# Performance work log

Hardware: AMD Instinct MI355X
Metric: run time of the kernel (lower is better)

## Reference

```python
import jax, jax.numpy as jnp
import numpy as np

N = 100000   # num nodes
E = 1600000  # num edges
D = 64       # feature / hidden dim (irreps_in == hidden_dim)
SCALE = D ** -0.5


def setup_inputs() -> dict:
    key = jax.random.key(0)
    ks = jax.random.split(key, 6)
    x = jax.random.normal(ks[0], (N, D), dtype=jnp.float32)
    edge_index = jax.random.randint(ks[1], (2, E), 0, N, dtype=jnp.int32)
    std = D ** -0.5
    Wq = jax.random.normal(ks[2], (D, D), dtype=jnp.float32) * std
    Wk = jax.random.normal(ks[3], (D, D), dtype=jnp.float32) * std
    Wv = jax.random.normal(ks[4], (D, D), dtype=jnp.float32) * std
    Wo = jax.random.normal(ks[5], (D, D), dtype=jnp.float32) * std
    return {"x": x, "edge_index": edge_index, "Wq": Wq, "Wk": Wk, "Wv": Wv, "Wo": Wo}


def reference(x, edge_index, Wq, Wk, Wv, Wo):
    # Per-receiver variable-length attention over incoming neighbors.
    # Mathematically identical to the torch module's degree-bucketed SDPA
    # (softmax over each node's neighbor set), without padding buffers.
    sender, receiver = edge_index[0], edge_index[1]
    Q = x @ Wq  # [N, D]
    K = x @ Wk
    V = x @ Wv
    # per-edge logits: <Q[receiver], K[sender]> * scale
    s = jnp.einsum('ed,ed->e', Q[receiver], K[sender]) * SCALE  # [E]
    # numerically stable segment softmax over receiver groups
    m = jax.ops.segment_max(s, receiver, num_segments=N)  # -inf for empty segments
    m_safe = jnp.where(jnp.isfinite(m), m, 0.0)
    p = jnp.exp(s - m_safe[receiver])  # [E]
    denom = jax.ops.segment_sum(p, receiver, num_segments=N)  # [N]
    num = jax.ops.segment_sum(p[:, None] * V[sender], receiver, num_segments=N)  # [N, D]
    # zero-degree nodes get out = 0 (matches torch: skipped buckets + nan_to_num)
    out = jnp.where(denom[:, None] > 0,
                    num / jnp.maximum(denom, 1e-30)[:, None],
                    0.0)
    return x + out @ Wo
```

## Files before the change

kernel.cpp:

```cpp
#include <hip/hip_runtime.h>
#include <hip/hip_bf16.h>

#define DIM 64
#define SCALE 0.125f
#define BINSH 5
#define NPB 32
#define BCAP 768
#define CHUNK 16384
#define MAXBINS 3200

static __device__ __forceinline__ unsigned int pack2bf(float a, float b) {
    unsigned int ua = __float_as_uint(a), ub = __float_as_uint(b);
    ua += 0x7fffu + ((ua >> 16) & 1u);
    ub += 0x7fffu + ((ub >> 16) & 1u);
    return (ua >> 16) | (ub & 0xffff0000u);
}
static __device__ __forceinline__ float2 unpack2bf(unsigned int u) {
    return make_float2(__uint_as_float(u << 16), __uint_as_float(u & 0xffff0000u));
}

__global__ __launch_bounds__(256) void k_fused(const int* __restrict__ send,
                                               const int* __restrict__ recv,
                                               const float* __restrict__ x,
                                               const float* __restrict__ Wq,
                                               const float* __restrict__ Wk,
                                               const float* __restrict__ Wv,
                                               const float* __restrict__ Wo,
                                               int* __restrict__ binCur,
                                               unsigned int* __restrict__ ebufA,
                                               float* __restrict__ Q,
                                               unsigned int* __restrict__ KVb,
                                               int E, int N, int NBK,
                                               int NBIN, int nchunk) {
    __shared__ __align__(16) float smem[20480];
    int tid = threadIdx.x;

    if ((int)blockIdx.x < NBIN) {
        int* hist = (int*)smem;
        int* lcur = hist + MAXBINS;
        int base = blockIdx.x * CHUNK;
        int lim = min(base + CHUNK, E);

        for (int i = tid; i < NBK; i += 256) hist[i] = 0;
        __syncthreads();
        for (int i = base + tid; i < lim; i += 256)
            atomicAdd(&hist[recv[i] >> BINSH], 1);
        __syncthreads();
        for (int i = tid; i < NBK; i += 256) {
            int h = hist[i];
            lcur[i] = h ? atomicAdd(&binCur[i], h) : 0;
        }
        __syncthreads();
        for (int i = base + tid; i < lim; i += 256) {
            int r = recv[i];
            int b = r >> BINSH;
            int p = atomicAdd(&lcur[b], 1);
            if (p < BCAP)
                ebufA[(size_t)b * BCAP + p] =
                    (unsigned)send[i] | ((unsigned)(r & (NPB - 1)) << 17);
        }
        return;
    }

    float* ws = smem;
    float* xs = smem + 4096;
    int wv = tid >> 6;
    int lane = tid & 63;
    int qb = blockIdx.x - NBIN;
    int m = qb / nchunk;
    int cb = qb % nchunk;

    if (m < 2) {
        const float* W = (m == 0) ? Wq : Wk;
        for (int i = tid; i < 1024; i += 256) ((float4*)ws)[i] = ((const float4*)W)[i];
        __syncthreads();
    } else {
        float* av = xs;
        float* bo = xs + 4096;
        for (int i = tid; i < 1024; i += 256) {
            ((float4*)av)[i] = ((const float4*)Wv)[i];
            ((float4*)bo)[i] = ((const float4*)Wo)[i];
        }
        __syncthreads();
        int r = tid >> 2, c0 = (tid & 3) * 16;
        float wvo[16];
#pragma unroll
        for (int j = 0; j < 16; j++) wvo[j] = 0.f;
        for (int k = 0; k < 64; k++) {
            float a = av[r * 64 + k];
#pragma unroll
            for (int j = 0; j < 16; j++)
                wvo[j] = fmaf(a, bo[k * 64 + c0 + j], wvo[j]);
        }
        __syncthreads();
#pragma unroll
        for (int j = 0; j < 16; j++) ws[r * 64 + c0 + j] = wvo[j];
        __syncthreads();
    }

    int base = cb * 256 + wv * 64;
    if (base < N) {
        float* xw = xs + wv * 4096;
#pragma unroll
        for (int c4 = 0; c4 < 16; c4++) {
            float4 v = make_float4(0.f, 0.f, 0.f, 0.f);
            if (base + lane < N) v = ((const float4*)x)[(size_t)(base + lane) * 16 + c4];
            xw[(c4 * 4 + 0) * 64 + lane] = v.x;
            xw[(c4 * 4 + 1) * 64 + lane] = v.y;
            xw[(c4 * 4 + 2) * 64 + lane] = v.z;
            xw[(c4 * 4 + 3) * 64 + lane] = v.w;
        }
        asm volatile("s_waitcnt lgkmcnt(0)" ::: "memory");

        int lr = lane >> 3;
        int lc = lane & 7;
        const float* xp = xw + lr * 8;
        const float* wp = ws + lc * 8;

        float acc[8][8];
#pragma unroll
        for (int i = 0; i < 8; i++)
#pragma unroll
            for (int j = 0; j < 8; j++) acc[i][j] = 0.f;

        float4 xa = *(const float4*)(xp);
        float4 xb = *(const float4*)(xp + 4);
        float4 wa = *(const float4*)(wp);
        float4 wb = *(const float4*)(wp + 4);
#pragma unroll 4
        for (int k = 0; k < 64; k++) {
            float4 xan, xbn, wan, wbn;
            if (k < 63) {
                xan = *(const float4*)(xp + (k + 1) * 64);
                xbn = *(const float4*)(xp + (k + 1) * 64 + 4);
                wan = *(const float4*)(wp + (k + 1) * 64);
                wbn = *(const float4*)(wp + (k + 1) * 64 + 4);
            }
            float xv[8] = {xa.x, xa.y, xa.z, xa.w, xb.x, xb.y, xb.z, xb.w};
            float wc[8] = {wa.x, wa.y, wa.z, wa.w, wb.x, wb.y, wb.z, wb.w};
#pragma unroll
            for (int i = 0; i < 8; i++)
#pragma unroll
                for (int j = 0; j < 8; j++)
                    acc[i][j] = fmaf(xv[i], wc[j], acc[i][j]);
            xa = xan; xb = xbn; wa = wan; wb = wbn;
        }

#pragma unroll
        for (int i = 0; i < 8; i++) {
            int row = base + lr * 8 + i;
            if (row < N) {
                if (m == 0) {
                    float* dst = &Q[(size_t)row * 64 + lc * 8];
                    ((float4*)dst)[0] = make_float4(acc[i][0], acc[i][1], acc[i][2], acc[i][3]);
                    ((float4*)dst)[1] = make_float4(acc[i][4], acc[i][5], acc[i][6], acc[i][7]);
                } else {
                    unsigned int* dst = &KVb[(size_t)row * 64 + (m - 1) * 32 + lc * 4];
                    uint4 pk;
                    pk.x = pack2bf(acc[i][0], acc[i][1]);
                    pk.y = pack2bf(acc[i][2], acc[i][3]);
                    pk.z = pack2bf(acc[i][4], acc[i][5]);
                    pk.w = pack2bf(acc[i][6], acc[i][7]);
                    *((uint4*)dst) = pk;
                }
            }
        }
    }
}

__global__ __launch_bounds__(256) void k_attn(const float* __restrict__ Q,
                                              const unsigned int* __restrict__ KVb,
                                              const float* __restrict__ x,
                                              const int* __restrict__ binCur,
                                              const unsigned int* __restrict__ ebufA,
                                              float* __restrict__ out, int N) {
    __shared__ unsigned int llist[BCAP];
    __shared__ int ldeg[NPB], lofs[NPB + 1], lcur[NPB];
    int tid = threadIdx.x;
    int wv = tid >> 6;
    int lane = tid & 63;
    int g = lane >> 3;
    int sub = lane & 7;

    int j = blockIdx.x;
    int cnt = min(binCur[j], BCAP);
    const unsigned int* ebin = ebufA + (size_t)j * BCAP;

    if (tid < NPB) ldeg[tid] = 0;
    __syncthreads();

    for (int i = tid; i < cnt; i += 256)
        atomicAdd(&ldeg[(ebin[i] >> 17) & (NPB - 1)], 1);
    __syncthreads();

    if (wv == 0 && lane < NPB) {
        int d = ldeg[lane];
        int s = d;
        for (int o = 1; o < NPB; o <<= 1) {
            int t = __shfl_up(s, o, NPB);
            if ((lane & (NPB - 1)) >= o) s += t;
        }
        lofs[lane + 1] = s;
        lcur[lane] = s - d;
        if (lane == 0) lofs[0] = 0;
    }
    __syncthreads();

    for (int i = tid; i < cnt; i += 256) {
        unsigned int u = ebin[i];
        int n = (u >> 17) & (NPB - 1);
        int p = atomicAdd(&lcur[n], 1);
        llist[p] = u & 0x1FFFFu;
    }
    __syncthreads();

    for (int n = wv; n < NPB; n += 4) {
        int r = (j << BINSH) + n;
        if (r >= N) break;
        int start = lofs[n];
        int end = lofs[n + 1];
        float4 qa = *((const float4*)&Q[(size_t)r * 64 + sub * 8]);
        float4 qb = *((const float4*)&Q[(size_t)r * 64 + sub * 8 + 4]);
        float q[8] = {qa.x, qa.y, qa.z, qa.w, qb.x, qb.y, qb.z, qb.w};
        float acc[8] = {0.f, 0.f, 0.f, 0.f, 0.f, 0.f, 0.f, 0.f};
        float dpart = 0.f;

        int eA = start + g;
        bool vA = eA < end;
        unsigned int sA = vA ? llist[eA] : 0u;
        uint4 kA = *((const uint4*)&KVb[(size_t)sA * 64 + sub * 4]);
        uint4 uA = *((const uint4*)&KVb[(size_t)sA * 64 + 32 + sub * 4]);
        int eB = start + 8 + g;
        bool vB = eB < end;
        unsigned int sB = vB ? llist[eB] : 0u;
        uint4 kB = *((const uint4*)&KVb[(size_t)sB * 64 + sub * 4]);
        uint4 uB = *((const uint4*)&KVb[(size_t)sB * 64 + 32 + sub * 4]);

        for (int bb = start; bb < end; bb += 8) {
            int eC = bb + 16 + g;
            bool vC = eC < end;
            unsigned int sC = vC ? llist[eC] : 0u;
            uint4 kC = *((const uint4*)&KVb[(size_t)sC * 64 + sub * 4]);
            uint4 uC = *((const uint4*)&KVb[(size_t)sC * 64 + 32 + sub * 4]);

            float2 k01 = unpack2bf(kA.x), k23 = unpack2bf(kA.y);
            float2 k45 = unpack2bf(kA.z), k67 = unpack2bf(kA.w);
            float dot = q[0] * k01.x + q[1] * k01.y + q[2] * k23.x + q[3] * k23.y
                      + q[4] * k45.x + q[5] * k45.y + q[6] * k67.x + q[7] * k67.y;
            dot += __shfl_xor(dot, 1);
            dot += __shfl_xor(dot, 2);
            dot += __shfl_xor(dot, 4);
            float w = vA ? __expf(dot * SCALE) : 0.f;

            float2 v01 = unpack2bf(uA.x), v23 = unpack2bf(uA.y);
            float2 v45 = unpack2bf(uA.z), v67 = unpack2bf(uA.w);
            acc[0] = fmaf(w, v01.x, acc[0]);
            acc[1] = fmaf(w, v01.y, acc[1]);
            acc[2] = fmaf(w, v23.x, acc[2]);
            acc[3] = fmaf(w, v23.y, acc[3]);
            acc[4] = fmaf(w, v45.x, acc[4]);
            acc[5] = fmaf(w, v45.y, acc[5]);
            acc[6] = fmaf(w, v67.x, acc[6]);
            acc[7] = fmaf(w, v67.y, acc[7]);
            dpart += w;

            kA = kB; uA = uB; vA = vB;
            kB = kC; uB = uC; vB = vC;
        }

        dpart += __shfl_xor(dpart, 8); dpart += __shfl_xor(dpart, 16); dpart += __shfl_xor(dpart, 32);
#pragma unroll
        for (int jj = 0; jj < 8; jj++) {
            acc[jj] += __shfl_xor(acc[jj], 8);
            acc[jj] += __shfl_xor(acc[jj], 16);
            acc[jj] += __shfl_xor(acc[jj], 32);
        }

        float inv = (dpart > 0.f) ? (1.0f / dpart) : 0.f;

        if (g == 0) {
            float4 xa = *((const float4*)&x[(size_t)r * 64 + sub * 8]);
            float4 xb = *((const float4*)&x[(size_t)r * 64 + sub * 8 + 4]);
            float4 oa = make_float4(fmaf(acc[0], inv, xa.x), fmaf(acc[1], inv, xa.y),
                                    fmaf(acc[2], inv, xa.z), fmaf(acc[3], inv, xa.w));
            float4 ob = make_float4(fmaf(acc[4], inv, xb.x), fmaf(acc[5], inv, xb.y),
                                    fmaf(acc[6], inv, xb.z), fmaf(acc[7], inv, xb.w));
            *((float4*)&out[(size_t)r * 64 + sub * 8]) = oa;
            *((float4*)&out[(size_t)r * 64 + sub * 8 + 4]) = ob;
        }
    }
}


extern "C" void kernel_launch(void* const* d_in, const int* in_sizes, int n_in,
                              void* d_out, int out_size, void* d_ws, size_t ws_size,
                              hipStream_t stream) {
    const float* x  = (const float*)d_in[0];
    const int* edge = (const int*)d_in[1];
    const float* Wq = (const float*)d_in[2];
    const float* Wk = (const float*)d_in[3];
    const float* Wv = (const float*)d_in[4];
    const float* Wo = (const float*)d_in[5];
    float* out = (float*)d_out;

    int N = in_sizes[0] / DIM;
    int E = in_sizes[1] / 2;
    int NBK = (N + NPB - 1) >> BINSH;

    char* p = (char*)d_ws;
    auto cv = [&](size_t bytes) {
        char* r = p;
        p += ((bytes + 255) / 256) * 256;
        return r;
    };
    float*        Q      = (float*)cv((size_t)N * 64 * 4);
    unsigned int* KVb    = (unsigned int*)cv((size_t)N * 64 * 4);
    int*          binCur = (int*)cv((size_t)NBK * 4);
    unsigned int* ebufA  = (unsigned int*)cv((size_t)NBK * BCAP * 4);
    (void)ws_size; (void)n_in; (void)out_size;

    const int* send = edge;
    const int* recv = edge + E;

    int NBIN = (E + CHUNK - 1) / CHUNK;
    int nchunk = (N + 255) / 256;

    hipMemsetAsync(binCur, 0, (size_t)NBK * 4, stream);
    k_fused<<<NBIN + 3 * nchunk, 256, 0, stream>>>(send, recv, x, Wq, Wk, Wv, Wo,
                                                   binCur, ebufA, Q, KVb,
                                                   E, N, NBK, NBIN, nchunk);
    k_attn<<<NBK, 256, 0, stream>>>(Q, KVb, x, binCur, ebufA, out, N);
}
```

Measured before the change: 241.7 us.

## Precompute Wv@Wo in separate kernel and read weights from global in projection

Moves the per-block Wv·Wo product into a single tiny kernel that runs once, instead of having every V-projection block recompute it. Projection blocks now read weight rows directly from global/L2, with a two-deep register prefetch, rather than staging them in shared memory. This cuts LDS per block from 80KB to 64KB. The binning chunk size is also halved to spread histogramming over more blocks. The trade-offs are an extra kernel launch and global-latency weight reads in the inner loop.

```diff
diff --git a/kernel.cpp b/kernel.cpp
--- a/kernel.cpp
+++ b/kernel.cpp
@@ -6,7 +6,7 @@
 #define BINSH 5
 #define NPB 32
 #define BCAP 768
-#define CHUNK 16384
+#define CHUNK 8192
 #define MAXBINS 3200
 
 static __device__ __forceinline__ unsigned int pack2bf(float a, float b) {
@@ -19,20 +19,44 @@
     return make_float2(__uint_as_float(u << 16), __uint_as_float(u & 0xffff0000u));
 }
 
+__global__ __launch_bounds__(256) void k_wmul(const float* __restrict__ Wv,
+                                              const float* __restrict__ Wo,
+                                              float* __restrict__ Wvo) {
+    __shared__ __align__(16) float av[64 * 64];
+    __shared__ __align__(16) float bo[64 * 64];
+    int tid = threadIdx.x;
+    for (int i = tid; i < 1024; i += 256) {
+        ((float4*)av)[i] = ((const float4*)Wv)[i];
+        ((float4*)bo)[i] = ((const float4*)Wo)[i];
+    }
+    __syncthreads();
+    int r = tid >> 2, c0 = (tid & 3) * 16;
+    float acc[16];
+#pragma unroll
+    for (int j = 0; j < 16; j++) acc[j] = 0.f;
+    for (int k = 0; k < 64; k++) {
+        float a = av[r * 64 + k];
+#pragma unroll
+        for (int j = 0; j < 16; j++)
+            acc[j] = fmaf(a, bo[k * 64 + c0 + j], acc[j]);
+    }
+#pragma unroll
+    for (int j = 0; j < 16; j++) Wvo[r * 64 + c0 + j] = acc[j];
+}
+
 __global__ __launch_bounds__(256) void k_fused(const int* __restrict__ send,
                                                const int* __restrict__ recv,
                                                const float* __restrict__ x,
                                                const float* __restrict__ Wq,
                                                const float* __restrict__ Wk,
-                                               const float* __restrict__ Wv,
-                                               const float* __restrict__ Wo,
+                                               const float* __restrict__ Wvo,
                                                int* __restrict__ binCur,
                                                unsigned int* __restrict__ ebufA,
                                                float* __restrict__ Q,
                                                unsigned int* __restrict__ KVb,
                                                int E, int N, int NBK,
                                                int NBIN, int nchunk) {
-    __shared__ __align__(16) float smem[20480];
+    __shared__ __align__(16) float smem[16384];
     int tid = threadIdx.x;
 
     if ((int)blockIdx.x < NBIN) {
@@ -62,45 +86,16 @@
         return;
     }
 
-    float* ws = smem;
-    float* xs = smem + 4096;
     int wv = tid >> 6;
     int lane = tid & 63;
     int qb = blockIdx.x - NBIN;
     int m = qb / nchunk;
     int cb = qb % nchunk;
-
-    if (m < 2) {
-        const float* W = (m == 0) ? Wq : Wk;
-        for (int i = tid; i < 1024; i += 256) ((float4*)ws)[i] = ((const float4*)W)[i];
-        __syncthreads();
-    } else {
-        float* av = xs;
-        float* bo = xs + 4096;
-        for (int i = tid; i < 1024; i += 256) {
-            ((float4*)av)[i] = ((const float4*)Wv)[i];
-            ((float4*)bo)[i] = ((const float4*)Wo)[i];
-        }
-        __syncthreads();
-        int r = tid >> 2, c0 = (tid & 3) * 16;
-        float wvo[16];
-#pragma unroll
-        for (int j = 0; j < 16; j++) wvo[j] = 0.f;
-        for (int k = 0; k < 64; k++) {
-            float a = av[r * 64 + k];
-#pragma unroll
-            for (int j = 0; j < 16; j++)
-                wvo[j] = fmaf(a, bo[k * 64 + c0 + j], wvo[j]);
-        }
-        __syncthreads();
-#pragma unroll
-        for (int j = 0; j < 16; j++) ws[r * 64 + c0 + j] = wvo[j];
-        __syncthreads();
-    }
+    const float* W = (m == 0) ? Wq : ((m == 1) ? Wk : Wvo);
 
     int base = cb * 256 + wv * 64;
     if (base < N) {
-        float* xw = xs + wv * 4096;
+        float* xw = smem + wv * 4096;
 #pragma unroll
         for (int c4 = 0; c4 < 16; c4++) {
             float4 v = make_float4(0.f, 0.f, 0.f, 0.f);
@@ -115,7 +110,7 @@
         int lr = lane >> 3;
         int lc = lane & 7;
         const float* xp = xw + lr * 8;
-        const float* wp = ws + lc * 8;
+        const float* wp = W + lc * 8;
 
         float acc[8][8];
 #pragma unroll
@@ -125,25 +120,31 @@
 
         float4 xa = *(const float4*)(xp);
         float4 xb = *(const float4*)(xp + 4);
-        float4 wa = *(const float4*)(wp);
-        float4 wb = *(const float4*)(wp + 4);
+        float4 wa0 = *(const float4*)(wp);
+        float4 wb0 = *(const float4*)(wp + 4);
+        float4 wa1 = *(const float4*)(wp + 64);
+        float4 wb1 = *(const float4*)(wp + 68);
 #pragma unroll 4
         for (int k = 0; k < 64; k++) {
             float4 xan, xbn, wan, wbn;
             if (k < 63) {
                 xan = *(const float4*)(xp + (k + 1) * 64);
                 xbn = *(const float4*)(xp + (k + 1) * 64 + 4);
-                wan = *(const float4*)(wp + (k + 1) * 64);
-                wbn = *(const float4*)(wp + (k + 1) * 64 + 4);
+            }
+            if (k < 62) {
+                wan = *(const float4*)(wp + (k + 2) * 64);
+                wbn = *(const float4*)(wp + (k + 2) * 64 + 4);
             }
             float xv[8] = {xa.x, xa.y, xa.z, xa.w, xb.x, xb.y, xb.z, xb.w};
-            float wc[8] = {wa.x, wa.y, wa.z, wa.w, wb.x, wb.y, wb.z, wb.w};
+            float wc[8] = {wa0.x, wa0.y, wa0.z, wa0.w, wb0.x, wb0.y, wb0.z, wb0.w};
 #pragma unroll
             for (int i = 0; i < 8; i++)
 #pragma unroll
                 for (int j = 0; j < 8; j++)
                     acc[i][j] = fmaf(xv[i], wc[j], acc[i][j]);
-            xa = xan; xb = xbn; wa = wan; wb = wbn;
+            xa = xan; xb = xbn;
+            wa0 = wa1; wb0 = wb1;
+            wa1 = wan; wb1 = wbn;
         }
 
 #pragma unroll
@@ -315,6 +316,7 @@
     };
     float*        Q      = (float*)cv((size_t)N * 64 * 4);
     unsigned int* KVb    = (unsigned int*)cv((size_t)N * 64 * 4);
+    float*        Wvo    = (float*)cv(64 * 64 * 4);
     int*          binCur = (int*)cv((size_t)NBK * 4);
     unsigned int* ebufA  = (unsigned int*)cv((size_t)NBK * BCAP * 4);
     (void)ws_size; (void)n_in; (void)out_size;
@@ -326,7 +328,8 @@
     int nchunk = (N + 255) / 256;
 
     hipMemsetAsync(binCur, 0, (size_t)NBK * 4, stream);
-    k_fused<<<NBIN + 3 * nchunk, 256, 0, stream>>>(send, recv, x, Wq, Wk, Wv, Wo,
+    k_wmul<<<1, 256, 0, stream>>>(Wv, Wo, Wvo);
+    k_fused<<<NBIN + 3 * nchunk, 256, 0, stream>>>(send, recv, x, Wq, Wk, Wvo,
                                                    binCur, ebufA, Q, KVb,
                                                    E, N, NBK, NBIN, nchunk);
     k_attn<<<NBK, 256, 0, stream>>>(Q, KVb, x, binCur, ebufA, out, N);
```

New measurement: 231.1 us. -4.4%, faster.
